# Kernel tuning notes

Hardware: AMD Instinct MI355X
Metric: run time of the kernel (lower is better)

The kernel has to match this reference:

```python
import jax, jax.numpy as jnp
import numpy as np

N_EMBD = 1024
NUM_EXPERTS = 8
TOP_K = 2


def new_gelu(x):
    # NewGELU: tanh approximation used by GPT-2
    c = jnp.sqrt(2.0 / jnp.pi).astype(x.dtype)
    return 0.5 * x * (1.0 + jnp.tanh(c * (x + 0.044715 * x ** 3)))


def setup_inputs() -> dict:
    key = jax.random.key(0)
    ks = jax.random.split(key, 6)
    C, E, H = N_EMBD, NUM_EXPERTS, 4 * N_EMBD
    x = jax.random.normal(ks[0], (4, 2048, C), dtype=jnp.float32)
    router_w = 0.02 * jax.random.normal(ks[1], (E, C), dtype=jnp.float32)  # Linear(C,E,bias=False).weight
    w1 = 0.02 * jax.random.normal(ks[2], (E, H, C), dtype=jnp.float32)     # c_fc.weight per expert
    b1 = jnp.zeros((E, H), dtype=jnp.float32)
    w2 = 0.02 * jax.random.normal(ks[3], (E, C, H), dtype=jnp.float32)     # c_proj.weight per expert
    b2 = jnp.zeros((E, C), dtype=jnp.float32)
    return {"x": x, "router_w": router_w, "w1": w1, "b1": b1, "w2": w2, "b2": b2}


def reference(x, router_w, w1, b1, w2, b2):
    B, T, C = x.shape
    E = router_w.shape[0]
    x_flat = x.reshape(B * T, C)  # [N, C]

    router_logits = x_flat @ router_w.T              # [N, E]
    router_probs = jax.nn.softmax(router_logits, axis=-1)
    top_k_probs, top_k_idx = jax.lax.top_k(router_probs, TOP_K)  # [N, K]
    top_k_probs = top_k_probs / (top_k_probs.sum(axis=-1, keepdims=True) + 1e-8)

    # combine weights per (token, expert): sum over k of gate_k * onehot(idx_k)
    cw = (jax.nn.one_hot(top_k_idx, E, dtype=x.dtype) * top_k_probs[..., None]).sum(axis=1)  # [N, E]

    output = jnp.zeros_like(x_flat)
    for e in range(E):  # small fixed expert count
        h = new_gelu(x_flat @ w1[e].T + b1[e])       # [N, 4C]
        out_e = h @ w2[e].T + b2[e]                  # [N, C]
        output = output + cw[:, e:e + 1] * out_e

    return output.reshape(B, T, C)
```

## Files before the change

### kernel.cpp

```cpp
#include <hip/hip_runtime.h>
#include <hip/hip_bf16.h>
#include <math.h>


#define N_TOK   8192
#define C_DIM   1024
#define H_DIM   4096
#define N_EXP   8
#define CAP     8192

typedef __bf16 bf16;
typedef bf16  bf16x8 __attribute__((ext_vector_type(8)));
typedef float f32x4  __attribute__((ext_vector_type(4)));

__device__ __forceinline__ void async_ld16(const void* g, void* l) {
    __builtin_amdgcn_global_load_lds(
        (const __attribute__((address_space(1))) void*)g,
        (__attribute__((address_space(3))) void*)l,
        16, 0, 0);
}

__device__ __forceinline__ float gelu_f(float v) {
    float u = v + 0.044715f * v * v * v;
    return 0.5f * v * (1.0f + tanhf(0.7978845608028654f * u));
}

__global__ void cvt_x_k(const float* __restrict__ x, bf16* __restrict__ xb, int n8) {
    int i = blockIdx.x * blockDim.x + threadIdx.x;
    if (i >= n8) return;
    const float4* p = (const float4*)x + (size_t)i * 2;
    float4 a = p[0], b = p[1];
    bf16x8 v;
    v[0] = (bf16)a.x; v[1] = (bf16)a.y; v[2] = (bf16)a.z; v[3] = (bf16)a.w;
    v[4] = (bf16)b.x; v[5] = (bf16)b.y; v[6] = (bf16)b.z; v[7] = (bf16)b.w;
    *((bf16x8*)xb + i) = v;
}

__global__ __launch_bounds__(1024) void router_k(const float* __restrict__ x,
                                                 const float* __restrict__ rw,
                                                 int* __restrict__ counts,
                                                 int* __restrict__ tok,
                                                 float* __restrict__ gate) {
    __shared__ int lcnt[N_EXP];
    __shared__ int lbase[N_EXP];
    const int tid  = threadIdx.x;
    const int lane = tid & 63;
    const int wv   = tid >> 6;
    if (tid < N_EXP) lcnt[tid] = 0;
    __syncthreads();

    const int t = blockIdx.x * 16 + wv;

    float dot[N_EXP];
#pragma unroll
    for (int e = 0; e < N_EXP; ++e) dot[e] = 0.f;
    const float4* xr = (const float4*)(x + (size_t)t * C_DIM);
#pragma unroll
    for (int j = 0; j < 4; ++j) {
        float4 xv = xr[j * 64 + lane];
#pragma unroll
        for (int e = 0; e < N_EXP; ++e) {
            float4 w4 = ((const float4*)(rw + (size_t)e * C_DIM))[j * 64 + lane];
            dot[e] += xv.x * w4.x + xv.y * w4.y + xv.z * w4.z + xv.w * w4.w;
        }
    }
#pragma unroll
    for (int e = 0; e < N_EXP; ++e) {
#pragma unroll
        for (int o = 32; o > 0; o >>= 1) dot[e] += __shfl_xor(dot[e], o, 64);
    }

    int a = 0, b = 0, ra = 0, rb = 0;
    float g0 = 0.f, g1 = 0.f;
    if (lane == 0) {
        float m = dot[0];
#pragma unroll
        for (int e = 1; e < N_EXP; ++e) m = fmaxf(m, dot[e]);
        float p[N_EXP]; float s = 0.f;
#pragma unroll
        for (int e = 0; e < N_EXP; ++e) { p[e] = expf(dot[e] - m); s += p[e]; }
        a = 0;
#pragma unroll
        for (int e = 1; e < N_EXP; ++e) if (p[e] > p[a]) a = e;
        b = -1;
#pragma unroll
        for (int e = 0; e < N_EXP; ++e) if (e != a && (b < 0 || p[e] > p[b])) b = e;
        float pa = p[a] / s, pb = p[b] / s;
        float d = pa + pb + 1e-8f;
        g0 = pa / d; g1 = pb / d;
        ra = atomicAdd(&lcnt[a], 1);
        rb = atomicAdd(&lcnt[b], 1);
    }
    __syncthreads();
    if (tid < N_EXP) lbase[tid] = atomicAdd(&counts[tid], lcnt[tid]);
    __syncthreads();
    if (lane == 0) {
        int sa = lbase[a] + ra;
        int sb = lbase[b] + rb;
        tok[a * CAP + sa] = t;  gate[a * CAP + sa] = g0;
        tok[b * CAP + sb] = t;  gate[b * CAP + sb] = g1;
    }
}

__global__ void prefix_k(const int* __restrict__ counts, int* __restrict__ offs) {
    if (threadIdx.x == 0) {
        int s = 0;
        for (int e = 0; e < N_EXP; ++e) { offs[e] = s; s += counts[e]; }
    }
}

__global__ __launch_bounds__(256) void fc1_k(const bf16* __restrict__ xb,
                                             const float* __restrict__ w1,
                                             const float* __restrict__ b1,
                                             const int* __restrict__ counts,
                                             const int* __restrict__ offs,
                                             const int* __restrict__ tok,
                                             bf16* __restrict__ h) {
    const int e   = blockIdx.z;
    const int cnt = counts[e];
    const int m0  = blockIdx.y * 128;
    if (m0 >= cnt) return;
    const int n0  = blockIdx.x * 128;
    const int off = offs[e];

    __shared__ __align__(16) bf16 As[128][32];
    __shared__ __align__(16) bf16 Bs[128][32];

    const int tid  = threadIdx.x;
    const int lane = tid & 63;
    const int wv   = tid >> 6;
    const int wm   = wv & 1;
    const int wn   = wv >> 1;

    const int ar0  = wv * 16 + (lane >> 2);
    const int ar1  = 64 + wv * 16 + (lane >> 2);
    const int acol = (lane & 3) * 8;
    const int i0 = m0 + ar0; const int i1 = m0 + ar1;
    const int t0 = tok[e * CAP + (i0 < cnt ? i0 : cnt - 1)];
    const int t1 = tok[e * CAP + (i1 < cnt ? i1 : cnt - 1)];
    const bf16* ga0 = xb + (size_t)t0 * C_DIM + acol;
    const bf16* ga1 = xb + (size_t)t1 * C_DIM + acol;
    bf16* la0 = &As[wv * 16][0];
    bf16* la1 = &As[64 + wv * 16][0];

    const int brow0 = tid >> 2;
    const int brow1 = 64 + (tid >> 2);
    const int bcol  = (tid & 3) * 8;
    const float* gb0 = w1 + ((size_t)e * H_DIM + n0 + brow0) * C_DIM + bcol;
    const float* gb1 = w1 + ((size_t)e * H_DIM + n0 + brow1) * C_DIM + bcol;

    f32x4 acc[4][4];
#pragma unroll
    for (int mi = 0; mi < 4; ++mi)
#pragma unroll
        for (int ni = 0; ni < 4; ++ni)
#pragma unroll
            for (int r = 0; r < 4; ++r) acc[mi][ni][r] = 0.f;

    for (int kt = 0; kt < C_DIM / 32; ++kt) {
        const int k0 = kt * 32;
        async_ld16(ga0 + k0, la0);
        async_ld16(ga1 + k0, la1);
        {
            float4 u0 = *(const float4*)(gb0 + k0);
            float4 u1 = *(const float4*)(gb0 + k0 + 4);
            bf16x8 v;
            v[0]=(bf16)u0.x; v[1]=(bf16)u0.y; v[2]=(bf16)u0.z; v[3]=(bf16)u0.w;
            v[4]=(bf16)u1.x; v[5]=(bf16)u1.y; v[6]=(bf16)u1.z; v[7]=(bf16)u1.w;
            *(bf16x8*)&Bs[brow0][bcol] = v;
            float4 u2 = *(const float4*)(gb1 + k0);
            float4 u3 = *(const float4*)(gb1 + k0 + 4);
            bf16x8 w;
            w[0]=(bf16)u2.x; w[1]=(bf16)u2.y; w[2]=(bf16)u2.z; w[3]=(bf16)u2.w;
            w[4]=(bf16)u3.x; w[5]=(bf16)u3.y; w[6]=(bf16)u3.z; w[7]=(bf16)u3.w;
            *(bf16x8*)&Bs[brow1][bcol] = w;
        }
        __syncthreads();

        bf16x8 af[4];
#pragma unroll
        for (int mi = 0; mi < 4; ++mi)
            af[mi] = *(const bf16x8*)&As[wm * 64 + mi * 16 + (lane & 15)][(lane >> 4) * 8];
#pragma unroll
        for (int ni = 0; ni < 4; ++ni) {
            bf16x8 bfr = *(const bf16x8*)&Bs[wn * 64 + ni * 16 + (lane & 15)][(lane >> 4) * 8];
#pragma unroll
            for (int mi = 0; mi < 4; ++mi)
                acc[mi][ni] = __builtin_amdgcn_mfma_f32_16x16x32_bf16(af[mi], bfr, acc[mi][ni], 0, 0, 0);
        }
        __syncthreads();
    }

    const int lg = lane >> 4, ln = lane & 15;
#pragma unroll
    for (int mi = 0; mi < 4; ++mi) {
#pragma unroll
        for (int r = 0; r < 4; ++r) {
            const int m = wm * 64 + mi * 16 + lg * 4 + r;
            if (m0 + m < cnt) {
                const size_t hrow = (size_t)(off + m0 + m) * H_DIM;
#pragma unroll
                for (int ni = 0; ni < 4; ++ni) {
                    const int n = n0 + wn * 64 + ni * 16 + ln;
                    float v = acc[mi][ni][r] + b1[(size_t)e * H_DIM + n];
                    h[hrow + n] = (bf16)gelu_f(v);
                }
            }
        }
    }
}

__global__ __launch_bounds__(256) void fc2_k(const bf16* __restrict__ h,
                                             const float* __restrict__ w2,
                                             const float* __restrict__ b2,
                                             const int* __restrict__ counts,
                                             const int* __restrict__ offs,
                                             const int* __restrict__ tok,
                                             const float* __restrict__ gate,
                                             float* __restrict__ out) {
    const int e   = blockIdx.z;
    const int cnt = counts[e];
    const int m0  = blockIdx.y * 128;
    if (m0 >= cnt) return;
    const int n0  = blockIdx.x * 128;
    const int off = offs[e];

    __shared__ __align__(16) bf16 As[128][32];
    __shared__ __align__(16) bf16 Bs[128][32];

    const int tid  = threadIdx.x;
    const int lane = tid & 63;
    const int wv   = tid >> 6;
    const int wm   = wv & 1;
    const int wn   = wv >> 1;

    const int ar0  = wv * 16 + (lane >> 2);
    const int ar1  = 64 + wv * 16 + (lane >> 2);
    const int acol = (lane & 3) * 8;
    const int i0 = m0 + ar0; const int i1 = m0 + ar1;
    const size_t hr0 = (size_t)(off + (i0 < cnt ? i0 : cnt - 1)) * H_DIM;
    const size_t hr1 = (size_t)(off + (i1 < cnt ? i1 : cnt - 1)) * H_DIM;
    const bf16* ga0 = h + hr0 + acol;
    const bf16* ga1 = h + hr1 + acol;
    bf16* la0 = &As[wv * 16][0];
    bf16* la1 = &As[64 + wv * 16][0];

    const int brow0 = tid >> 2;
    const int brow1 = 64 + (tid >> 2);
    const int bcol  = (tid & 3) * 8;
    const float* gb0 = w2 + ((size_t)e * C_DIM + n0 + brow0) * H_DIM + bcol;
    const float* gb1 = w2 + ((size_t)e * C_DIM + n0 + brow1) * H_DIM + bcol;

    f32x4 acc[4][4];
#pragma unroll
    for (int mi = 0; mi < 4; ++mi)
#pragma unroll
        for (int ni = 0; ni < 4; ++ni)
#pragma unroll
            for (int r = 0; r < 4; ++r) acc[mi][ni][r] = 0.f;

    for (int kt = 0; kt < H_DIM / 32; ++kt) {
        const int k0 = kt * 32;
        async_ld16(ga0 + k0, la0);
        async_ld16(ga1 + k0, la1);
        {
            float4 u0 = *(const float4*)(gb0 + k0);
            float4 u1 = *(const float4*)(gb0 + k0 + 4);
            bf16x8 v;
            v[0]=(bf16)u0.x; v[1]=(bf16)u0.y; v[2]=(bf16)u0.z; v[3]=(bf16)u0.w;
            v[4]=(bf16)u1.x; v[5]=(bf16)u1.y; v[6]=(bf16)u1.z; v[7]=(bf16)u1.w;
            *(bf16x8*)&Bs[brow0][bcol] = v;
            float4 u2 = *(const float4*)(gb1 + k0);
            float4 u3 = *(const float4*)(gb1 + k0 + 4);
            bf16x8 w;
            w[0]=(bf16)u2.x; w[1]=(bf16)u2.y; w[2]=(bf16)u2.z; w[3]=(bf16)u2.w;
            w[4]=(bf16)u3.x; w[5]=(bf16)u3.y; w[6]=(bf16)u3.z; w[7]=(bf16)u3.w;
            *(bf16x8*)&Bs[brow1][bcol] = w;
        }
        __syncthreads();

        bf16x8 af[4];
#pragma unroll
        for (int mi = 0; mi < 4; ++mi)
            af[mi] = *(const bf16x8*)&As[wm * 64 + mi * 16 + (lane & 15)][(lane >> 4) * 8];
#pragma unroll
        for (int ni = 0; ni < 4; ++ni) {
            bf16x8 bfr = *(const bf16x8*)&Bs[wn * 64 + ni * 16 + (lane & 15)][(lane >> 4) * 8];
#pragma unroll
            for (int mi = 0; mi < 4; ++mi)
                acc[mi][ni] = __builtin_amdgcn_mfma_f32_16x16x32_bf16(af[mi], bfr, acc[mi][ni], 0, 0, 0);
        }
        __syncthreads();
    }

    const int lg = lane >> 4, ln = lane & 15;
#pragma unroll
    for (int mi = 0; mi < 4; ++mi) {
#pragma unroll
        for (int r = 0; r < 4; ++r) {
            const int m = wm * 64 + mi * 16 + lg * 4 + r;
            if (m0 + m < cnt) {
                const int   tk = tok[e * CAP + m0 + m];
                const float g  = gate[e * CAP + m0 + m];
#pragma unroll
                for (int ni = 0; ni < 4; ++ni) {
                    const int n = n0 + wn * 64 + ni * 16 + ln;
                    float v = (acc[mi][ni][r] + b2[(size_t)e * C_DIM + n]) * g;
                    atomicAdd(&out[(size_t)tk * C_DIM + n], v);
                }
            }
        }
    }
}

extern "C" void kernel_launch(void* const* d_in, const int* in_sizes, int n_in,
                              void* d_out, int out_size, void* d_ws, size_t ws_size,
                              hipStream_t stream) {
    const float* x  = (const float*)d_in[0];
    const float* rw = (const float*)d_in[1];
    const float* w1 = (const float*)d_in[2];
    const float* b1 = (const float*)d_in[3];
    const float* w2 = (const float*)d_in[4];
    const float* b2 = (const float*)d_in[5];
    float* out = (float*)d_out;

    char* ws = (char*)d_ws;
    size_t o = 0;
    bf16* xb     = (bf16*)(ws + o);  o += (size_t)N_TOK * C_DIM * sizeof(bf16);
    int*  tok    = (int*)(ws + o);   o += (size_t)N_EXP * CAP * sizeof(int);
    float* gate  = (float*)(ws + o); o += (size_t)N_EXP * CAP * sizeof(float);
    int*  counts = (int*)(ws + o);   o += 128;
    int*  offs   = (int*)(ws + o);   o += 128;
    bf16* h      = (bf16*)(ws + o);  o += (size_t)(2 * N_TOK) * H_DIM * sizeof(bf16);

    hipMemsetAsync(d_out, 0, (size_t)N_TOK * C_DIM * sizeof(float), stream);
    hipMemsetAsync(counts, 0, 128, stream);

    cvt_x_k<<<dim3((N_TOK * C_DIM / 8 + 255) / 256), dim3(256), 0, stream>>>(x, xb, N_TOK * C_DIM / 8);
    router_k<<<dim3(N_TOK / 16), dim3(1024), 0, stream>>>(x, rw, counts, tok, gate);
    prefix_k<<<dim3(1), dim3(64), 0, stream>>>(counts, offs);
    fc1_k<<<dim3(H_DIM / 128, N_TOK / 128, N_EXP), dim3(256), 0, stream>>>(xb, w1, b1, counts, offs, tok, h);
    fc2_k<<<dim3(C_DIM / 128, N_TOK / 128, N_EXP), dim3(256), 0, stream>>>(h, w2, b2, counts, offs, tok, gate, out);
}
```

Measured before the change: 977.7 us.

## Pre-convert expert weights to bf16 and load them asynchronously with swizzled LDS

Adds per-call kernels that convert w1 and w2 from fp32 to bf16 in workspace. The GEMM kernels can then stream both operands with async global-to-LDS loads instead of per-tile fp32 loads and in-register conversion. It also XOR-swizzles LDS column placement to reduce bank conflicts on fragment reads. The trade is an extra conversion pass over 64M weights on every call (256MB read, 128MB written), in exchange for halving the weight bytes each GEMM tile re-reads.

```diff
diff --git a/kernel.cpp b/kernel.cpp
--- a/kernel.cpp
+++ b/kernel.cpp
@@ -25,15 +25,15 @@
     return 0.5f * v * (1.0f + tanhf(0.7978845608028654f * u));
 }
 
-__global__ void cvt_x_k(const float* __restrict__ x, bf16* __restrict__ xb, int n8) {
+__global__ void cvt_k(const float* __restrict__ src, bf16* __restrict__ dst, int n8) {
     int i = blockIdx.x * blockDim.x + threadIdx.x;
     if (i >= n8) return;
-    const float4* p = (const float4*)x + (size_t)i * 2;
+    const float4* p = (const float4*)src + (size_t)i * 2;
     float4 a = p[0], b = p[1];
     bf16x8 v;
     v[0] = (bf16)a.x; v[1] = (bf16)a.y; v[2] = (bf16)a.z; v[3] = (bf16)a.w;
     v[4] = (bf16)b.x; v[5] = (bf16)b.y; v[6] = (bf16)b.z; v[7] = (bf16)b.w;
-    *((bf16x8*)xb + i) = v;
+    *((bf16x8*)dst + i) = v;
 }
 
 __global__ __launch_bounds__(1024) void router_k(const float* __restrict__ x,
@@ -109,8 +109,9 @@
     }
 }
 
+
 __global__ __launch_bounds__(256) void fc1_k(const bf16* __restrict__ xb,
-                                             const float* __restrict__ w1,
+                                             const bf16* __restrict__ w1b,
                                              const float* __restrict__ b1,
                                              const int* __restrict__ counts,
                                              const int* __restrict__ offs,
@@ -132,22 +133,22 @@
     const int wm   = wv & 1;
     const int wn   = wv >> 1;
 
-    const int ar0  = wv * 16 + (lane >> 2);
-    const int ar1  = 64 + wv * 16 + (lane >> 2);
-    const int acol = (lane & 3) * 8;
-    const int i0 = m0 + ar0; const int i1 = m0 + ar1;
+    const int scol = (((lane & 3) ^ ((lane >> 3) & 3))) * 8;
+
+    const int ar0 = wv * 16 + (lane >> 2);
+    const int ar1 = 64 + wv * 16 + (lane >> 2);
+    const int i0 = m0 + ar0, i1 = m0 + ar1;
     const int t0 = tok[e * CAP + (i0 < cnt ? i0 : cnt - 1)];
     const int t1 = tok[e * CAP + (i1 < cnt ? i1 : cnt - 1)];
-    const bf16* ga0 = xb + (size_t)t0 * C_DIM + acol;
-    const bf16* ga1 = xb + (size_t)t1 * C_DIM + acol;
+    const bf16* ga0 = xb + (size_t)t0 * C_DIM + scol;
+    const bf16* ga1 = xb + (size_t)t1 * C_DIM + scol;
     bf16* la0 = &As[wv * 16][0];
     bf16* la1 = &As[64 + wv * 16][0];
 
-    const int brow0 = tid >> 2;
-    const int brow1 = 64 + (tid >> 2);
-    const int bcol  = (tid & 3) * 8;
-    const float* gb0 = w1 + ((size_t)e * H_DIM + n0 + brow0) * C_DIM + bcol;
-    const float* gb1 = w1 + ((size_t)e * H_DIM + n0 + brow1) * C_DIM + bcol;
+    const bf16* gb0 = w1b + ((size_t)e * H_DIM + n0 + ar0) * C_DIM + scol;
+    const bf16* gb1 = w1b + ((size_t)e * H_DIM + n0 + ar1) * C_DIM + scol;
+    bf16* lb0 = &Bs[wv * 16][0];
+    bf16* lb1 = &Bs[64 + wv * 16][0];
 
     f32x4 acc[4][4];
 #pragma unroll
@@ -156,34 +157,26 @@
         for (int ni = 0; ni < 4; ++ni)
 #pragma unroll
             for (int r = 0; r < 4; ++r) acc[mi][ni][r] = 0.f;
+
+    const int r_   = lane & 15;
+    const int g_   = lane >> 4;
+    const int rcol = (g_ ^ ((r_ >> 1) & 3)) * 8;
 
     for (int kt = 0; kt < C_DIM / 32; ++kt) {
         const int k0 = kt * 32;
         async_ld16(ga0 + k0, la0);
         async_ld16(ga1 + k0, la1);
-        {
-            float4 u0 = *(const float4*)(gb0 + k0);
-            float4 u1 = *(const float4*)(gb0 + k0 + 4);
-            bf16x8 v;
-            v[0]=(bf16)u0.x; v[1]=(bf16)u0.y; v[2]=(bf16)u0.z; v[3]=(bf16)u0.w;
-            v[4]=(bf16)u1.x; v[5]=(bf16)u1.y; v[6]=(bf16)u1.z; v[7]=(bf16)u1.w;
-            *(bf16x8*)&Bs[brow0][bcol] = v;
-            float4 u2 = *(const float4*)(gb1 + k0);
-            float4 u3 = *(const float4*)(gb1 + k0 + 4);
-            bf16x8 w;
-            w[0]=(bf16)u2.x; w[1]=(bf16)u2.y; w[2]=(bf16)u2.z; w[3]=(bf16)u2.w;
-            w[4]=(bf16)u3.x; w[5]=(bf16)u3.y; w[6]=(bf16)u3.z; w[7]=(bf16)u3.w;
-            *(bf16x8*)&Bs[brow1][bcol] = w;
-        }
+        async_ld16(gb0 + k0, lb0);
+        async_ld16(gb1 + k0, lb1);
         __syncthreads();
 
         bf16x8 af[4];
 #pragma unroll
         for (int mi = 0; mi < 4; ++mi)
-            af[mi] = *(const bf16x8*)&As[wm * 64 + mi * 16 + (lane & 15)][(lane >> 4) * 8];
+            af[mi] = *(const bf16x8*)&As[wm * 64 + mi * 16 + r_][rcol];
 #pragma unroll
         for (int ni = 0; ni < 4; ++ni) {
-            bf16x8 bfr = *(const bf16x8*)&Bs[wn * 64 + ni * 16 + (lane & 15)][(lane >> 4) * 8];
+            bf16x8 bfr = *(const bf16x8*)&Bs[wn * 64 + ni * 16 + r_][rcol];
 #pragma unroll
             for (int mi = 0; mi < 4; ++mi)
                 acc[mi][ni] = __builtin_amdgcn_mfma_f32_16x16x32_bf16(af[mi], bfr, acc[mi][ni], 0, 0, 0);
@@ -211,7 +204,7 @@
 }
 
 __global__ __launch_bounds__(256) void fc2_k(const bf16* __restrict__ h,
-                                             const float* __restrict__ w2,
+                                             const bf16* __restrict__ w2b,
                                              const float* __restrict__ b2,
                                              const int* __restrict__ counts,
                                              const int* __restrict__ offs,
@@ -234,22 +227,22 @@
     const int wm   = wv & 1;
     const int wn   = wv >> 1;
 
-    const int ar0  = wv * 16 + (lane >> 2);
-    const int ar1  = 64 + wv * 16 + (lane >> 2);
-    const int acol = (lane & 3) * 8;
-    const int i0 = m0 + ar0; const int i1 = m0 + ar1;
+    const int scol = (((lane & 3) ^ ((lane >> 3) & 3))) * 8;
+
+    const int ar0 = wv * 16 + (lane >> 2);
+    const int ar1 = 64 + wv * 16 + (lane >> 2);
+    const int i0 = m0 + ar0, i1 = m0 + ar1;
     const size_t hr0 = (size_t)(off + (i0 < cnt ? i0 : cnt - 1)) * H_DIM;
     const size_t hr1 = (size_t)(off + (i1 < cnt ? i1 : cnt - 1)) * H_DIM;
-    const bf16* ga0 = h + hr0 + acol;
-    const bf16* ga1 = h + hr1 + acol;
+    const bf16* ga0 = h + hr0 + scol;
+    const bf16* ga1 = h + hr1 + scol;
     bf16* la0 = &As[wv * 16][0];
     bf16* la1 = &As[64 + wv * 16][0];
 
-    const int brow0 = tid >> 2;
-    const int brow1 = 64 + (tid >> 2);
-    const int bcol  = (tid & 3) * 8;
-    const float* gb0 = w2 + ((size_t)e * C_DIM + n0 + brow0) * H_DIM + bcol;
-    const float* gb1 = w2 + ((size_t)e * C_DIM + n0 + brow1) * H_DIM + bcol;
+    const bf16* gb0 = w2b + ((size_t)e * C_DIM + n0 + ar0) * H_DIM + scol;
+    const bf16* gb1 = w2b + ((size_t)e * C_DIM + n0 + ar1) * H_DIM + scol;
+    bf16* lb0 = &Bs[wv * 16][0];
+    bf16* lb1 = &Bs[64 + wv * 16][0];
 
     f32x4 acc[4][4];
 #pragma unroll
@@ -258,34 +251,26 @@
         for (int ni = 0; ni < 4; ++ni)
 #pragma unroll
             for (int r = 0; r < 4; ++r) acc[mi][ni][r] = 0.f;
+
+    const int r_   = lane & 15;
+    const int g_   = lane >> 4;
+    const int rcol = (g_ ^ ((r_ >> 1) & 3)) * 8;
 
     for (int kt = 0; kt < H_DIM / 32; ++kt) {
         const int k0 = kt * 32;
         async_ld16(ga0 + k0, la0);
         async_ld16(ga1 + k0, la1);
-        {
-            float4 u0 = *(const float4*)(gb0 + k0);
-            float4 u1 = *(const float4*)(gb0 + k0 + 4);
-            bf16x8 v;
-            v[0]=(bf16)u0.x; v[1]=(bf16)u0.y; v[2]=(bf16)u0.z; v[3]=(bf16)u0.w;
-            v[4]=(bf16)u1.x; v[5]=(bf16)u1.y; v[6]=(bf16)u1.z; v[7]=(bf16)u1.w;
-            *(bf16x8*)&Bs[brow0][bcol] = v;
-            float4 u2 = *(const float4*)(gb1 + k0);
-            float4 u3 = *(const float4*)(gb1 + k0 + 4);
-            bf16x8 w;
-            w[0]=(bf16)u2.x; w[1]=(bf16)u2.y; w[2]=(bf16)u2.z; w[3]=(bf16)u2.w;
-            w[4]=(bf16)u3.x; w[5]=(bf16)u3.y; w[6]=(bf16)u3.z; w[7]=(bf16)u3.w;
-            *(bf16x8*)&Bs[brow1][bcol] = w;
-        }
+        async_ld16(gb0 + k0, lb0);
+        async_ld16(gb1 + k0, lb1);
         __syncthreads();
 
         bf16x8 af[4];
 #pragma unroll
         for (int mi = 0; mi < 4; ++mi)
-            af[mi] = *(const bf16x8*)&As[wm * 64 + mi * 16 + (lane & 15)][(lane >> 4) * 8];
+            af[mi] = *(const bf16x8*)&As[wm * 64 + mi * 16 + r_][rcol];
 #pragma unroll
         for (int ni = 0; ni < 4; ++ni) {
-            bf16x8 bfr = *(const bf16x8*)&Bs[wn * 64 + ni * 16 + (lane & 15)][(lane >> 4) * 8];
+            bf16x8 bfr = *(const bf16x8*)&Bs[wn * 64 + ni * 16 + r_][rcol];
 #pragma unroll
             for (int mi = 0; mi < 4; ++mi)
                 acc[mi][ni] = __builtin_amdgcn_mfma_f32_16x16x32_bf16(af[mi], bfr, acc[mi][ni], 0, 0, 0);
@@ -327,6 +312,8 @@
     char* ws = (char*)d_ws;
     size_t o = 0;
     bf16* xb     = (bf16*)(ws + o);  o += (size_t)N_TOK * C_DIM * sizeof(bf16);
+    bf16* w1b    = (bf16*)(ws + o);  o += (size_t)N_EXP * H_DIM * C_DIM * sizeof(bf16);
+    bf16* w2b    = (bf16*)(ws + o);  o += (size_t)N_EXP * C_DIM * H_DIM * sizeof(bf16);
     int*  tok    = (int*)(ws + o);   o += (size_t)N_EXP * CAP * sizeof(int);
     float* gate  = (float*)(ws + o); o += (size_t)N_EXP * CAP * sizeof(float);
     int*  counts = (int*)(ws + o);   o += 128;
@@ -336,9 +323,12 @@
     hipMemsetAsync(d_out, 0, (size_t)N_TOK * C_DIM * sizeof(float), stream);
     hipMemsetAsync(counts, 0, 128, stream);
 
-    cvt_x_k<<<dim3((N_TOK * C_DIM / 8 + 255) / 256), dim3(256), 0, stream>>>(x, xb, N_TOK * C_DIM / 8);
+    const int NW = N_EXP * H_DIM * C_DIM / 8;
+    cvt_k<<<dim3((N_TOK * C_DIM / 8 + 255) / 256), 256, 0, stream>>>(x, xb, N_TOK * C_DIM / 8);
+    cvt_k<<<dim3((NW + 255) / 256), 256, 0, stream>>>(w1, w1b, NW);
+    cvt_k<<<dim3((NW + 255) / 256), 256, 0, stream>>>(w2, w2b, NW);
     router_k<<<dim3(N_TOK / 16), dim3(1024), 0, stream>>>(x, rw, counts, tok, gate);
     prefix_k<<<dim3(1), dim3(64), 0, stream>>>(counts, offs);
-    fc1_k<<<dim3(H_DIM / 128, N_TOK / 128, N_EXP), dim3(256), 0, stream>>>(xb, w1, b1, counts, offs, tok, h);
-    fc2_k<<<dim3(C_DIM / 128, N_TOK / 128, N_EXP), dim3(256), 0, stream>>>(h, w2, b2, counts, offs, tok, gate, out);
-}
+    fc1_k<<<dim3(H_DIM / 128, N_TOK / 128, N_EXP), dim3(256), 0, stream>>>(xb, w1b, b1, counts, offs, tok, h);
+    fc2_k<<<dim3(C_DIM / 128, N_TOK / 128, N_EXP), dim3(256), 0, stream>>>(h, w2b, b2, counts, offs, tok, gate, out);
+}
```

After: 908.5 us. 1.08x faster.
